# Kernel tuning notes

Measured on AMD Instinct MI355X. Metric: run time of the kernel, lower is better.

The kernel has to match this reference:

```python
import jax, jax.numpy as jnp
import numpy as np

STRIDE = 1
PAD = 1
EXTENT = 3  # kernel footprint (ceil of max tap offset), 3x3 tap grid


def setup_inputs() -> dict:
    key = jax.random.key(0)
    k1, k2 = jax.random.split(key)
    B, Cin, H, W = 8, 64, 128, 128
    Cout, K = 64, 9
    x = jax.random.normal(k1, (B, Cin, H, W), dtype=jnp.float32)
    # per-tap weights, one scalar weight per (out_ch, in_ch, tap) -- op formula is 'x * w'
    weights = jax.random.normal(k2, (Cout, Cin, K), dtype=jnp.float32) * 0.05
    # 3x3 integer grid shifted by +0.4 -> non-integer offsets => bilinear (sub-pixel) gather
    base = jnp.stack(jnp.meshgrid(jnp.arange(3.0), jnp.arange(3.0), indexing='ij'), -1).reshape(9, 2)
    tap_offsets = (base + 0.4).astype(jnp.float32)  # [K, 2] (dy, dx)
    return {"x": x, "weights": weights, "tap_offsets": tap_offsets}


def _bilinear_tap(xp, dy, dx, H_out, W_out):
    # Gather xp at (oy*stride + dy, ox*stride + dx) with separable bilinear interp.
    Hp, Wp = xp.shape[-2], xp.shape[-1]
    y = jnp.arange(H_out, dtype=xp.dtype) * STRIDE + dy
    xc = jnp.arange(W_out, dtype=xp.dtype) * STRIDE + dx
    y0 = jnp.floor(y)
    x0 = jnp.floor(xc)
    fy = (y - y0)[None, None, :, None]
    fx = (xc - x0)[None, None, None, :]
    y0i = jnp.clip(y0.astype(jnp.int32), 0, Hp - 1)
    y1i = jnp.clip(y0.astype(jnp.int32) + 1, 0, Hp - 1)
    x0i = jnp.clip(x0.astype(jnp.int32), 0, Wp - 1)
    x1i = jnp.clip(x0.astype(jnp.int32) + 1, 0, Wp - 1)
    # interp rows first: [B, C, H_out, Wp]
    ry = xp[:, :, y0i, :] * (1.0 - fy) + xp[:, :, y1i, :] * fy
    # then columns: [B, C, H_out, W_out]
    return ry[:, :, :, x0i] * (1.0 - fx) + ry[:, :, :, x1i] * fx


def reference(x, weights, tap_offsets):
    B, Cin, H, W = x.shape
    K = weights.shape[-1]
    xp = jnp.pad(x, ((0, 0), (0, 0), (PAD, PAD), (PAD, PAD)))
    H_out = (H + 2 * PAD - EXTENT) // STRIDE + 1
    W_out = (W + 2 * PAD - EXTENT) // STRIDE + 1
    # gather all taps (loop over small fixed K=9, each fully vectorized over B,C,H,W)
    taps = [_bilinear_tap(xp, tap_offsets[k, 0], tap_offsets[k, 1], H_out, W_out)
            for k in range(K)]
    g = jnp.stack(taps, 0)  # [K, B, Cin, H_out, W_out]
    # per-tap op 'x * w', accumulated over taps and input channels
    return jnp.einsum('kbiyx,oik->boyx', g, weights)  # [B, Cout, H_out, W_out]
```

## Files before the change

kernel.cpp:

```cpp
#include <hip/hip_runtime.h>


#define CIN   64
#define COUT  64
#define HH    128
#define WW    128

typedef __attribute__((ext_vector_type(8)))  short bf16x8;
typedef __attribute__((ext_vector_type(4)))  float f32x4;
typedef __attribute__((ext_vector_type(16))) float f32x16;
typedef __attribute__((ext_vector_type(4)))  unsigned int u32x4;

__device__ __forceinline__ unsigned short f2bf(float f) {
  unsigned int u = __float_as_uint(f);
  u = (u + 0x7fffu + ((u >> 16) & 1u)) >> 16;
  return (unsigned short)u;
}

__global__ void make_wb(const float* __restrict__ wgt,
                        const float* __restrict__ off,
                        unsigned short* __restrict__ wb)
{
  int id = blockIdx.x * 64 + threadIdx.x;
  int o = id >> 6, c = id & 63;
  float W16[16];
  #pragma unroll
  for (int i = 0; i < 16; ++i) W16[i] = 0.f;
  for (int k = 0; k < 9; ++k) {
    float dy = off[2*k], dx = off[2*k+1];
    float fyf = floorf(dy), fxf = floorf(dx);
    int   iy = (int)fyf,   ix = (int)fxf;
    float fy = dy - fyf,   fx = dx - fxf;
    float wk = wgt[(o*CIN + c)*9 + k];
    W16[(iy  )*4 + ix  ] += wk * (1.f-fy)*(1.f-fx);
    W16[(iy  )*4 + ix+1] += wk * (1.f-fy)*fx;
    W16[(iy+1)*4 + ix  ] += wk * fy*(1.f-fx);
    W16[(iy+1)*4 + ix+1] += wk * fy*fx;
  }
  int g = c >> 4, half = (c >> 3) & 1, j = c & 7;
  int ni = o >> 5, l31 = o & 31;
  int lane = half*32 + l31;
  for (int tap = 0; tap < 16; ++tap) {
    int h8 = tap >> 3, rs8 = tap & 7;
    wb[(size_t)((((g*2 + h8)*16) + rs8*2 + ni)*64 + lane)*8 + j] = f2bf(W16[tap]);
  }
}

constexpr int CELL = 72;
constexpr int LPOS = 68;

__global__ __launch_bounds__(256, 2)
void conv_mfma(const float* __restrict__ x,
               const unsigned short* __restrict__ wb,
               float* __restrict__ out)
{
  __shared__ unsigned short lt[7 * LPOS * CELL];

  const int wg = blockIdx.x;
  const int b  = wg >> 6;
  const int y0 = ((wg >> 1) & 31) * 4;
  const int x0 = (wg & 1) * 64;
  const int t  = threadIdx.x;

  for (int id = t; id < 56 * LPOS; id += 256) {
    int cg  = id / LPOS;
    int pos = id - cg * LPOS;
    int row = cg >> 3;
    int c8  = cg & 7;
    int gy  = y0 + row - 1;
    int gx  = x0 + pos - 1;
    bool ok = ((unsigned)gy < (unsigned)HH) && ((unsigned)gx < (unsigned)WW);
    int sgy = ok ? gy : 0, sgx = ok ? gx : 0;
    float sc = ok ? 1.f : 0.f;
    const float* ps = x + ((size_t)(b*CIN + c8*8)*HH + sgy)*WW + sgx;
    float v[8];
    #pragma unroll
    for (int cc = 0; cc < 8; ++cc) v[cc] = ps[(size_t)cc*HH*WW] * sc;
    unsigned int pk[4];
    #pragma unroll
    for (int i = 0; i < 4; ++i)
      pk[i] = (unsigned int)f2bf(v[2*i]) | ((unsigned int)f2bf(v[2*i+1]) << 16);
    *(u32x4*)&lt[(row*LPOS + pos)*CELL + c8*8] = *(u32x4*)pk;
  }
  __syncthreads();

  const int lane = t & 63;
  const int wave = t >> 6;
  const int l31  = lane & 31;
  const int half = lane >> 5;

  f32x16 acc[2][2];
  #pragma unroll
  for (int xh = 0; xh < 2; ++xh)
    #pragma unroll
    for (int ni = 0; ni < 2; ++ni)
      acc[xh][ni] = (f32x16)(0.f);

  const unsigned short* wl = wb + lane*8;

  #pragma unroll
  for (int g = 0; g < 4; ++g) {
    #pragma unroll
    for (int h8 = 0; h8 < 2; ++h8) {
      bf16x8 bfr[8][2];
      #pragma unroll
      for (int rs8 = 0; rs8 < 8; ++rs8)
        #pragma unroll
        for (int ni = 0; ni < 2; ++ni)
          bfr[rs8][ni] = *(const bf16x8*)(wl + (size_t)(((g*2 + h8)*16) + rs8*2 + ni)*512);
      #pragma unroll
      for (int rs8 = 0; rs8 < 8; ++rs8) {
        const int tap = h8*8 + rs8;
        const int r = tap >> 2, sx = tap & 3;
        #pragma unroll
        for (int xh = 0; xh < 2; ++xh) {
          bf16x8 afr = *(const bf16x8*)
            &lt[((wave + r)*LPOS + (xh*32 + l31 + sx))*CELL + g*16 + half*8];
          acc[xh][0] = __builtin_amdgcn_mfma_f32_32x32x16_bf16(afr, bfr[rs8][0], acc[xh][0], 0, 0, 0);
          acc[xh][1] = __builtin_amdgcn_mfma_f32_32x32x16_bf16(afr, bfr[rs8][1], acc[xh][1], 0, 0, 0);
        }
      }
    }
  }

  const int y = y0 + wave;
  #pragma unroll
  for (int xh = 0; xh < 2; ++xh) {
    #pragma unroll
    for (int ni = 0; ni < 2; ++ni) {
      int o = ni*32 + l31;
      float* dst = out + (((size_t)(b*COUT + o))*HH + y)*WW + x0 + xh*32 + 4*half;
      #pragma unroll
      for (int rg = 0; rg < 4; ++rg) {
        f32x4 v = (f32x4){acc[xh][ni][4*rg+0], acc[xh][ni][4*rg+1],
                          acc[xh][ni][4*rg+2], acc[xh][ni][4*rg+3]};
        *(f32x4*)(dst + 8*rg) = v;
      }
    }
  }
}

extern "C" void kernel_launch(void* const* d_in, const int* in_sizes, int n_in,
                              void* d_out, int out_size, void* d_ws, size_t ws_size,
                              hipStream_t stream)
{
  const float* x   = (const float*)d_in[0];
  const float* wgt = (const float*)d_in[1];
  const float* off = (const float*)d_in[2];
  float* out = (float*)d_out;
  unsigned short* wb = (unsigned short*)d_ws;

  make_wb<<<64, 64, 0, stream>>>(wgt, off, wb);
  conv_mfma<<<512, 256, 0, stream>>>(x, wb, out);
}
```

Before: 116.8 us.

## Split input channels into two LDS phases and double-buffer weight fragments

Stages the input tile into LDS in two halves of 32 channels instead of all 64 at once. This cuts the shared-memory footprint to roughly 38KB, so launch bounds can request 3 workgroups per CU. Weight fragments are now loaded in small groups and prefetched one step ahead, replacing the large 16-fragment register buffer, which lowers register pressure. The cost is an extra barrier and a second staging pass per block, with less overlap between the global loads and the MFMA work.

```diff
diff --git a/kernel.cpp b/kernel.cpp
--- a/kernel.cpp
+++ b/kernel.cpp
@@ -46,44 +46,21 @@
   }
 }
 
-constexpr int CELL = 72;
-constexpr int LPOS = 68;
+constexpr int CELLS = 40;
+constexpr int LPOS  = 68;
 
-__global__ __launch_bounds__(256, 2)
+__global__ __launch_bounds__(256, 3)
 void conv_mfma(const float* __restrict__ x,
                const unsigned short* __restrict__ wb,
                float* __restrict__ out)
 {
-  __shared__ unsigned short lt[7 * LPOS * CELL];
+  __shared__ unsigned short lt[7 * LPOS * CELLS];
 
   const int wg = blockIdx.x;
   const int b  = wg >> 6;
   const int y0 = ((wg >> 1) & 31) * 4;
   const int x0 = (wg & 1) * 64;
   const int t  = threadIdx.x;
-
-  for (int id = t; id < 56 * LPOS; id += 256) {
-    int cg  = id / LPOS;
-    int pos = id - cg * LPOS;
-    int row = cg >> 3;
-    int c8  = cg & 7;
-    int gy  = y0 + row - 1;
-    int gx  = x0 + pos - 1;
-    bool ok = ((unsigned)gy < (unsigned)HH) && ((unsigned)gx < (unsigned)WW);
-    int sgy = ok ? gy : 0, sgx = ok ? gx : 0;
-    float sc = ok ? 1.f : 0.f;
-    const float* ps = x + ((size_t)(b*CIN + c8*8)*HH + sgy)*WW + sgx;
-    float v[8];
-    #pragma unroll
-    for (int cc = 0; cc < 8; ++cc) v[cc] = ps[(size_t)cc*HH*WW] * sc;
-    unsigned int pk[4];
-    #pragma unroll
-    for (int i = 0; i < 4; ++i)
-      pk[i] = (unsigned int)f2bf(v[2*i]) | ((unsigned int)f2bf(v[2*i+1]) << 16);
-    *(u32x4*)&lt[(row*LPOS + pos)*CELL + c8*8] = *(u32x4*)pk;
-  }
-  __syncthreads();
-
   const int lane = t & 63;
   const int wave = t >> 6;
   const int l31  = lane & 31;
@@ -99,27 +76,67 @@
   const unsigned short* wl = wb + lane*8;
 
   #pragma unroll
-  for (int g = 0; g < 4; ++g) {
-    #pragma unroll
-    for (int h8 = 0; h8 < 2; ++h8) {
-      bf16x8 bfr[8][2];
+  for (int p = 0; p < 2; ++p) {
+    if (p) __syncthreads();
+
+    for (int id = t; id < 28 * LPOS; id += 256) {
+      int cg  = id / LPOS;
+      int pos = id - cg * LPOS;
+      int row = cg >> 2;
+      int c8  = cg & 3;
+      int gy  = y0 + row - 1;
+      int gx  = x0 + pos - 1;
+      bool ok = ((unsigned)gy < (unsigned)HH) && ((unsigned)gx < (unsigned)WW);
+      int sgy = ok ? gy : 0, sgx = ok ? gx : 0;
+      float sc = ok ? 1.f : 0.f;
+      const float* ps = x + ((size_t)(b*CIN + p*32 + c8*8)*HH + sgy)*WW + sgx;
+      float v[8];
       #pragma unroll
-      for (int rs8 = 0; rs8 < 8; ++rs8)
+      for (int cc = 0; cc < 8; ++cc) v[cc] = ps[(size_t)cc*HH*WW] * sc;
+      unsigned int pk[4];
+      #pragma unroll
+      for (int i = 0; i < 4; ++i)
+        pk[i] = (unsigned int)f2bf(v[2*i]) | ((unsigned int)f2bf(v[2*i+1]) << 16);
+      *(u32x4*)&lt[(row*LPOS + pos)*CELLS + c8*8] = *(u32x4*)pk;
+    }
+    __syncthreads();
+
+    bf16x8 bcur[4], bnxt[4];
+    {
+      const int g = p*2;
+      #pragma unroll
+      for (int dt = 0; dt < 2; ++dt)
         #pragma unroll
         for (int ni = 0; ni < 2; ++ni)
-          bfr[rs8][ni] = *(const bf16x8*)(wl + (size_t)(((g*2 + h8)*16) + rs8*2 + ni)*512);
+          bcur[dt*2+ni] = *(const bf16x8*)(wl + (size_t)(((g*2 + 0)*16) + dt*2 + ni)*512);
+    }
+    #pragma unroll
+    for (int ki = 0; ki < 16; ++ki) {
+      if (ki < 15) {
+        const int kn = ki + 1;
+        const int g2n = kn >> 3, h8n = (kn >> 2) & 1, q4n = kn & 3;
+        const int gn = p*2 + g2n;
+        #pragma unroll
+        for (int dt = 0; dt < 2; ++dt)
+          #pragma unroll
+          for (int ni = 0; ni < 2; ++ni)
+            bnxt[dt*2+ni] = *(const bf16x8*)(wl + (size_t)(((gn*2 + h8n)*16) + (q4n*2+dt)*2 + ni)*512);
+      }
+      const int g2 = ki >> 3, h8 = (ki >> 2) & 1, q4 = ki & 3;
       #pragma unroll
-      for (int rs8 = 0; rs8 < 8; ++rs8) {
-        const int tap = h8*8 + rs8;
+      for (int dt = 0; dt < 2; ++dt) {
+        const int tap = h8*8 + q4*2 + dt;
         const int r = tap >> 2, sx = tap & 3;
         #pragma unroll
         for (int xh = 0; xh < 2; ++xh) {
           bf16x8 afr = *(const bf16x8*)
-            &lt[((wave + r)*LPOS + (xh*32 + l31 + sx))*CELL + g*16 + half*8];
-          acc[xh][0] = __builtin_amdgcn_mfma_f32_32x32x16_bf16(afr, bfr[rs8][0], acc[xh][0], 0, 0, 0);
-          acc[xh][1] = __builtin_amdgcn_mfma_f32_32x32x16_bf16(afr, bfr[rs8][1], acc[xh][1], 0, 0, 0);
+            &lt[((wave + r)*LPOS + (xh*32 + l31 + sx))*CELLS + g2*16 + half*8];
+          acc[xh][0] = __builtin_amdgcn_mfma_f32_32x32x16_bf16(afr, bcur[dt*2+0], acc[xh][0], 0, 0, 0);
+          acc[xh][1] = __builtin_amdgcn_mfma_f32_32x32x16_bf16(afr, bcur[dt*2+1], acc[xh][1], 0, 0, 0);
         }
       }
+      #pragma unroll
+      for (int i = 0; i < 4; ++i) bcur[i] = bnxt[i];
     }
   }
 
```

After: 116.2 us. No clear change (-0.6%).

## Pre-transpose input to padded bf16 channel-last buffer and stream MFMA operands from global

Applied to the files above, without the earlier changes.

Adds a separate kernel that converts x to a zero-padded, channel-grouped bf16 layout in workspace. The conv kernel drops its shared-memory staging and barrier and instead loads A and B fragments straight from global or L2, double-buffering one tap ahead in registers. The block-to-batch mapping is also reordered so neighbouring blocks cover different batches. This removes the strided fp32 gather and LDS traffic but adds an extra launch, a round trip of the transposed tensor through memory, and per-MFMA global load latency.

```diff
diff --git a/kernel.cpp b/kernel.cpp
--- a/kernel.cpp
+++ b/kernel.cpp
@@ -46,94 +46,120 @@
   }
 }
 
-constexpr int CELL = 72;
-constexpr int LPOS = 68;
+__global__ __launch_bounds__(128)
+void transpose_x(const float* __restrict__ x, unsigned short* __restrict__ xt)
+{
+  const int bid = blockIdx.x;
+  const int b   = bid / 131;
+  const int yp  = bid - b * 131;
+  const int t   = threadIdx.x;
 
-__global__ __launch_bounds__(256, 2)
-void conv_mfma(const float* __restrict__ x,
-               const unsigned short* __restrict__ wb,
-               float* __restrict__ out)
-{
-  __shared__ unsigned short lt[7 * LPOS * CELL];
+  unsigned short* rowbase = xt + (size_t)(b*132 + yp)*8*132*8;
 
-  const int wg = blockIdx.x;
-  const int b  = wg >> 6;
-  const int y0 = ((wg >> 1) & 31) * 4;
-  const int x0 = (wg & 1) * 64;
-  const int t  = threadIdx.x;
-
-  for (int id = t; id < 56 * LPOS; id += 256) {
-    int cg  = id / LPOS;
-    int pos = id - cg * LPOS;
-    int row = cg >> 3;
-    int c8  = cg & 7;
-    int gy  = y0 + row - 1;
-    int gx  = x0 + pos - 1;
-    bool ok = ((unsigned)gy < (unsigned)HH) && ((unsigned)gx < (unsigned)WW);
-    int sgy = ok ? gy : 0, sgx = ok ? gx : 0;
-    float sc = ok ? 1.f : 0.f;
-    const float* ps = x + ((size_t)(b*CIN + c8*8)*HH + sgy)*WW + sgx;
+  if (yp == 0 || yp >= 129) {
+    for (int i = t; i < 8*132; i += 128)
+      *(u32x4*)&rowbase[i*8] = (u32x4){0u,0u,0u,0u};
+    return;
+  }
+  const int gy = yp - 1;
+  const int px = t;
+  #pragma unroll
+  for (int cq = 0; cq < 8; ++cq) {
+    const float* ps = x + ((size_t)(b*CIN + cq*8)*HH + gy)*WW + px;
     float v[8];
     #pragma unroll
-    for (int cc = 0; cc < 8; ++cc) v[cc] = ps[(size_t)cc*HH*WW] * sc;
+    for (int cc = 0; cc < 8; ++cc) v[cc] = ps[(size_t)cc*HH*WW];
     unsigned int pk[4];
     #pragma unroll
     for (int i = 0; i < 4; ++i)
       pk[i] = (unsigned int)f2bf(v[2*i]) | ((unsigned int)f2bf(v[2*i+1]) << 16);
-    *(u32x4*)&lt[(row*LPOS + pos)*CELL + c8*8] = *(u32x4*)pk;
+    *(u32x4*)&rowbase[(cq*132 + px + 1)*8] = *(u32x4*)pk;
   }
-  __syncthreads();
+  if (t < 32) {
+    int cq = t >> 2, csel = t & 3;
+    int col = (csel == 0) ? 0 : (128 + csel);
+    *(u32x4*)&rowbase[(cq*132 + col)*8] = (u32x4){0u,0u,0u,0u};
+  }
+}
 
+__global__ __launch_bounds__(256, 2)
+void conv_mfma(const unsigned short* __restrict__ xt,
+               const unsigned short* __restrict__ wb,
+               float* __restrict__ out)
+{
+  const int wg = blockIdx.x;
+  const int b  = wg & 7;
+  const int i6 = wg >> 3;
+  const int y0 = (i6 >> 1) * 4;
+  const int x0 = (i6 & 1) * 64;
+  const int t  = threadIdx.x;
   const int lane = t & 63;
   const int wave = t >> 6;
   const int l31  = lane & 31;
   const int half = lane >> 5;
+  const int y    = y0 + wave;
 
   f32x16 acc[2][2];
   #pragma unroll
-  for (int xh = 0; xh < 2; ++xh)
+  for (int mi = 0; mi < 2; ++mi)
     #pragma unroll
     for (int ni = 0; ni < 2; ++ni)
-      acc[xh][ni] = (f32x16)(0.f);
+      acc[mi][ni] = (f32x16)(0.f);
 
   const unsigned short* wl = wb + lane*8;
+
+  const unsigned short* xbase = xt + (size_t)(b*132 + y)*8*132*8
+                                   + (size_t)(x0 + l31)*8 + (size_t)half*132*8;
+
+  bf16x8 aq[2][2], bq[2][2];
+
+  auto loadB = [&](int g, int tap, bf16x8 (&dst)[2]) {
+    int h8 = tap >> 3, rs8 = tap & 7;
+    #pragma unroll
+    for (int ni = 0; ni < 2; ++ni)
+      dst[ni] = *(const bf16x8*)(wl + (size_t)(((g*2 + h8)*16) + rs8*2 + ni)*512);
+  };
+  auto loadA = [&](int g, int tap, bf16x8 (&dst)[2]) {
+    int r = tap >> 2, s = tap & 3;
+    const unsigned short* p = xbase + (size_t)(r*8*132 + g*2*132 + s)*8;
+    #pragma unroll
+    for (int mi = 0; mi < 2; ++mi)
+      dst[mi] = *(const bf16x8*)(p + mi*32*8);
+  };
+
+  loadA(0, 0, aq[0]);
+  loadB(0, 0, bq[0]);
 
   #pragma unroll
   for (int g = 0; g < 4; ++g) {
     #pragma unroll
-    for (int h8 = 0; h8 < 2; ++h8) {
-      bf16x8 bfr[8][2];
+    for (int tap = 0; tap < 16; ++tap) {
+      if (tap < 15) {
+        loadA(g, tap + 1, aq[(tap + 1) & 1]);
+        loadB(g, tap + 1, bq[(tap + 1) & 1]);
+      } else if (g < 3) {
+        loadA(g + 1, 0, aq[0]);
+        loadB(g + 1, 0, bq[0]);
+      }
+      const int sl = tap & 1;
       #pragma unroll
-      for (int rs8 = 0; rs8 < 8; ++rs8)
-        #pragma unroll
-        for (int ni = 0; ni < 2; ++ni)
-          bfr[rs8][ni] = *(const bf16x8*)(wl + (size_t)(((g*2 + h8)*16) + rs8*2 + ni)*512);
-      #pragma unroll
-      for (int rs8 = 0; rs8 < 8; ++rs8) {
-        const int tap = h8*8 + rs8;
-        const int r = tap >> 2, sx = tap & 3;
-        #pragma unroll
-        for (int xh = 0; xh < 2; ++xh) {
-          bf16x8 afr = *(const bf16x8*)
-            &lt[((wave + r)*LPOS + (xh*32 + l31 + sx))*CELL + g*16 + half*8];
-          acc[xh][0] = __builtin_amdgcn_mfma_f32_32x32x16_bf16(afr, bfr[rs8][0], acc[xh][0], 0, 0, 0);
-          acc[xh][1] = __builtin_amdgcn_mfma_f32_32x32x16_bf16(afr, bfr[rs8][1], acc[xh][1], 0, 0, 0);
-        }
+      for (int mi = 0; mi < 2; ++mi) {
+        acc[mi][0] = __builtin_amdgcn_mfma_f32_32x32x16_bf16(aq[sl][mi], bq[sl][0], acc[mi][0], 0, 0, 0);
+        acc[mi][1] = __builtin_amdgcn_mfma_f32_32x32x16_bf16(aq[sl][mi], bq[sl][1], acc[mi][1], 0, 0, 0);
       }
     }
   }
 
-  const int y = y0 + wave;
   #pragma unroll
-  for (int xh = 0; xh < 2; ++xh) {
+  for (int mi = 0; mi < 2; ++mi) {
     #pragma unroll
     for (int ni = 0; ni < 2; ++ni) {
       int o = ni*32 + l31;
-      float* dst = out + (((size_t)(b*COUT + o))*HH + y)*WW + x0 + xh*32 + 4*half;
+      float* dst = out + (((size_t)(b*COUT + o))*HH + y)*WW + x0 + mi*32 + 4*half;
       #pragma unroll
       for (int rg = 0; rg < 4; ++rg) {
-        f32x4 v = (f32x4){acc[xh][ni][4*rg+0], acc[xh][ni][4*rg+1],
-                          acc[xh][ni][4*rg+2], acc[xh][ni][4*rg+3]};
+        f32x4 v = (f32x4){acc[mi][ni][4*rg+0], acc[mi][ni][4*rg+1],
+                          acc[mi][ni][4*rg+2], acc[mi][ni][4*rg+3]};
         *(f32x4*)(dst + 8*rg) = v;
       }
     }
@@ -148,8 +174,11 @@
   const float* wgt = (const float*)d_in[1];
   const float* off = (const float*)d_in[2];
   float* out = (float*)d_out;
+
   unsigned short* wb = (unsigned short*)d_ws;
+  unsigned short* xt = (unsigned short*)d_ws + 65536;
 
   make_wb<<<64, 64, 0, stream>>>(wgt, off, wb);
-  conv_mfma<<<512, 256, 0, stream>>>(x, wb, out);
+  transpose_x<<<8*131, 128, 0, stream>>>(x, xt);
+  conv_mfma<<<512, 256, 0, stream>>>(xt, wb, out);
 }
```

Result: slower. 125.3 us (+7.3%).
